# Kernel optimization log

Measured on AMD Instinct MI355X. Metric: run time of the kernel, lower is better.

The kernel has to match this reference:

```python
import jax, jax.numpy as jnp
import numpy as np

RING_SIZE = 4
SEGMENT_LEN = 1024
DILATION_RATE = 2
EPS = 1e-8


def setup_inputs() -> dict:
    key = jax.random.key(0)
    kq, kk, kv = jax.random.split(key, 3)
    shape = (1, 4096, 16, 64)  # (b, n, h, d)
    q = jax.random.normal(kq, shape, dtype=jnp.float32)
    k = jax.random.normal(kk, shape, dtype=jnp.float32)
    v = jax.random.normal(kv, shape, dtype=jnp.float32)
    return {"q": q, "k": k, "v": v}


def _gather_dilated_chunks(k_local, v_local, chunk_size):
    """Replicate the ring loop: rank 0, dist not initialized -> KV chunk is
    always the local chunk; only the dilation offset varies per ring step.
    Returns concatenated dilated K, V of total length ring_size*chunk_size."""
    ks, vs = [], []
    base = jnp.arange(chunk_size)
    for step in range(RING_SIZE):
        chunk_rank = (-step) % RING_SIZE
        chunk_start = chunk_rank * chunk_size
        offset = (chunk_start // SEGMENT_LEN) % DILATION_RATE
        if DILATION_RATE == 1:
            idx = base
        else:
            idx = (base * DILATION_RATE + offset) % chunk_size
        ks.append(k_local[:, idx])
        vs.append(v_local[:, idx])
    return jnp.concatenate(ks, axis=1), jnp.concatenate(vs, axis=1)


def reference(q, k, v):
    b, n, h, d = q.shape
    chunk_size = n // RING_SIZE
    k_local = k[:, :chunk_size]  # rank 0 local chunk
    v_local = v[:, :chunk_size]
    K, V = _gather_dilated_chunks(k_local, v_local, chunk_size)  # (b, n, h, d)

    # Online softmax over ring steps is mathematically a single stable softmax
    # over the concatenation of all chunk scores, with +1e-8 on sum_exp.
    scale = 1.0 / jnp.sqrt(jnp.asarray(d, dtype=q.dtype))
    scores = jnp.einsum("bqhd,bkhd->bhqk", q, K) * scale  # (b, h, n, n)
    m = jnp.max(scores, axis=-1, keepdims=True)
    p = jnp.exp(scores - m)
    denom = jnp.sum(p, axis=-1, keepdims=True) + EPS  # (b, h, q, 1)
    out = jnp.einsum("bhqk,bkhd->bqhd", p, V)  # (b, q, h, d)
    out = out / jnp.transpose(denom, (0, 2, 1, 3))  # -> (b, q, h, 1)
    return out
```

## Files before the change

kernel.cpp:

```cpp
#include <hip/hip_runtime.h>


typedef __attribute__((ext_vector_type(8))) _Float16 f16x8;
typedef __attribute__((ext_vector_type(2))) __fp16   h16x2;
typedef __attribute__((ext_vector_type(4))) float    f32x4;
typedef __attribute__((ext_vector_type(4))) int      i32x4;

constexpr int HEADS = 16;
constexpr int NQ    = 4096;
constexpr int NK    = 1024;
constexpr int KB    = 64;
constexpr int NT    = NK / KB;
constexpr int NTW   = NT / 2;

constexpr int IMG_K  = 0;
constexpr int IMG_V  = 8192;
constexpr int IMG_SZ = 16384;

constexpr float KSCALE = 0.18033688011112042f;
constexpr float CINIT  = -2.8853900817779268f;

__global__ __launch_bounds__(256)
void prepass(const float* __restrict__ kg, const float* __restrict__ vg,
             char* __restrict__ ws)
{
    const int kt = blockIdx.x;
    const int h  = blockIdx.y;
    const int kb = kt * KB;
    char* img = ws + (size_t)(h * NT + kt) * IMG_SZ;
    const int tid = threadIdx.x;

    #pragma unroll
    for (int i = 0; i < 2; ++i) {
        int u = i * 256 + tid;
        int f = u >> 6, l = u & 63;
        int t = f >> 1, cc = f & 1;
        int g = l >> 4, c = l & 15;
        const float* src = kg + (size_t)(kb + 16 * t + c) * 1024 + h * 64 + 32 * cc + 8 * g;
        float4 a = *(const float4*)src;
        float4 b = *(const float4*)(src + 4);
        f16x8 kk;
        kk[0] = (_Float16)(a.x * KSCALE); kk[1] = (_Float16)(a.y * KSCALE);
        kk[2] = (_Float16)(a.z * KSCALE); kk[3] = (_Float16)(a.w * KSCALE);
        kk[4] = (_Float16)(b.x * KSCALE); kk[5] = (_Float16)(b.y * KSCALE);
        kk[6] = (_Float16)(b.z * KSCALE); kk[7] = (_Float16)(b.w * KSCALE);
        *(f16x8*)(img + IMG_K + u * 16) = kk;
    }

    #pragma unroll
    for (int i = 0; i < 2; ++i) {
        int u = i * 256 + tid;
        int f = u >> 6, l = u & 63;
        int m = f >> 2, td = f & 3;
        int g = l >> 4, c = l & 15;
        f16x8 vv;
        #pragma unroll
        for (int e = 0; e < 8; ++e) {
            int key = kb + 32 * m + 16 * (e >> 2) + 4 * g + (e & 3);
            vv[e] = (_Float16)vg[(size_t)key * 1024 + h * 64 + 16 * td + c];
        }
        *(f16x8*)(img + IMG_V + u * 16) = vv;
    }
}

__global__ __launch_bounds__(128, 2)
void ring_attn_v24(const float* __restrict__ qg,
                   const char* __restrict__ ws,
                   float* __restrict__ outg)
{
    __shared__ __align__(16) float Ob[64 * 68 + 64];

    const int bid  = blockIdx.x;
    const int xcd  = bid & 7;
    const int slot = bid >> 3;
    const int h    = xcd * 2 + (slot >> 6);
    const int qw   = slot & 63;

    const int tid  = threadIdx.x;
    const int w    = tid >> 6;
    const int lane = tid & 63;
    const int g    = lane >> 4;
    const int c    = lane & 15;
    const int qbase = qw * 64;

    const int rot  = ((bid >> 3) ^ (w << 2)) & 7;

    f16x8 qf[4][2];
    #pragma unroll
    for (int H = 0; H < 4; ++H)
        #pragma unroll
        for (int cc = 0; cc < 2; ++cc) {
            const float* src = qg + (size_t)(qbase + 16 * H + c) * 1024 + h * 64 + 32 * cc + 8 * g;
            float4 a = *(const float4*)src;
            float4 b = *(const float4*)(src + 4);
            f16x8 qq;
            qq[0] = (_Float16)a.x; qq[1] = (_Float16)a.y;
            qq[2] = (_Float16)a.z; qq[3] = (_Float16)a.w;
            qq[4] = (_Float16)b.x; qq[5] = (_Float16)b.y;
            qq[6] = (_Float16)b.z; qq[7] = (_Float16)b.w;
            qf[H][cc] = qq;
        }

    const f32x4 cinit = {CINIT, CINIT, CINIT, CINIT};
    const h16x2 ones2 = {(__fp16)1.f, (__fp16)1.f};

    f32x4 o[4][4];
    #pragma unroll
    for (int H = 0; H < 4; ++H)
        #pragma unroll
        for (int td = 0; td < 4; ++td)
            #pragma unroll
            for (int r = 0; r < 4; ++r) o[H][td][r] = 0.f;
    float lac[4] = {0.f, 0.f, 0.f, 0.f};

    const char* himg = ws + (size_t)h * NT * IMG_SZ + lane * 16;

    #pragma unroll
    for (int i = 0; i < NTW; ++i) {
        const int kt = w * NTW + ((i + rot) & 7);
        const char* img = himg + (size_t)kt * IMG_SZ;

        f16x8 kv[8];
        #pragma unroll
        for (int f = 0; f < 8; ++f)
            kv[f] = *(const f16x8*)(img + IMG_K + f * 1024);

        f32x4 s0[4], s1[4], s2[4], s3[4];
        unsigned int wv[4][4][2];
        __builtin_amdgcn_s_setprio(1);
        #pragma unroll
        for (int t = 0; t < 4; ++t) {
            s0[t] = __builtin_amdgcn_mfma_f32_16x16x32_f16(kv[2 * t],     qf[0][0], cinit, 0, 0, 0);
            s0[t] = __builtin_amdgcn_mfma_f32_16x16x32_f16(kv[2 * t + 1], qf[0][1], s0[t], 0, 0, 0);
            s1[t] = __builtin_amdgcn_mfma_f32_16x16x32_f16(kv[2 * t],     qf[1][0], cinit, 0, 0, 0);
            s1[t] = __builtin_amdgcn_mfma_f32_16x16x32_f16(kv[2 * t + 1], qf[1][1], s1[t], 0, 0, 0);
        }
        __builtin_amdgcn_s_setprio(0);
        #pragma unroll
        for (int t = 0; t < 4; ++t) {
            float p0 = __builtin_amdgcn_exp2f(s0[t][0]);
            float p1 = __builtin_amdgcn_exp2f(s0[t][1]);
            float p2 = __builtin_amdgcn_exp2f(s0[t][2]);
            float p3 = __builtin_amdgcn_exp2f(s0[t][3]);
            h16x2 w0 = __builtin_amdgcn_cvt_pkrtz(p0, p1);
            h16x2 w1 = __builtin_amdgcn_cvt_pkrtz(p2, p3);
            lac[0] = __builtin_amdgcn_fdot2(w0, ones2, lac[0], false);
            lac[0] = __builtin_amdgcn_fdot2(w1, ones2, lac[0], false);
            wv[0][t][0] = __builtin_bit_cast(unsigned int, w0);
            wv[0][t][1] = __builtin_bit_cast(unsigned int, w1);
        }
        #pragma unroll
        for (int t = 0; t < 4; ++t) {
            float p0 = __builtin_amdgcn_exp2f(s1[t][0]);
            float p1 = __builtin_amdgcn_exp2f(s1[t][1]);
            float p2 = __builtin_amdgcn_exp2f(s1[t][2]);
            float p3 = __builtin_amdgcn_exp2f(s1[t][3]);
            h16x2 w0 = __builtin_amdgcn_cvt_pkrtz(p0, p1);
            h16x2 w1 = __builtin_amdgcn_cvt_pkrtz(p2, p3);
            lac[1] = __builtin_amdgcn_fdot2(w0, ones2, lac[1], false);
            lac[1] = __builtin_amdgcn_fdot2(w1, ones2, lac[1], false);
            wv[1][t][0] = __builtin_bit_cast(unsigned int, w0);
            wv[1][t][1] = __builtin_bit_cast(unsigned int, w1);
        }

        __builtin_amdgcn_s_setprio(1);
        #pragma unroll
        for (int t = 0; t < 4; ++t) {
            s2[t] = __builtin_amdgcn_mfma_f32_16x16x32_f16(kv[2 * t],     qf[2][0], cinit, 0, 0, 0);
            s2[t] = __builtin_amdgcn_mfma_f32_16x16x32_f16(kv[2 * t + 1], qf[2][1], s2[t], 0, 0, 0);
            s3[t] = __builtin_amdgcn_mfma_f32_16x16x32_f16(kv[2 * t],     qf[3][0], cinit, 0, 0, 0);
            s3[t] = __builtin_amdgcn_mfma_f32_16x16x32_f16(kv[2 * t + 1], qf[3][1], s3[t], 0, 0, 0);
        }
        __builtin_amdgcn_s_setprio(0);

        #pragma unroll
        for (int f = 0; f < 8; ++f)
            kv[f] = *(const f16x8*)(img + IMG_V + f * 1024);

        #pragma unroll
        for (int t = 0; t < 4; ++t) {
            float p0 = __builtin_amdgcn_exp2f(s2[t][0]);
            float p1 = __builtin_amdgcn_exp2f(s2[t][1]);
            float p2 = __builtin_amdgcn_exp2f(s2[t][2]);
            float p3 = __builtin_amdgcn_exp2f(s2[t][3]);
            h16x2 w0 = __builtin_amdgcn_cvt_pkrtz(p0, p1);
            h16x2 w1 = __builtin_amdgcn_cvt_pkrtz(p2, p3);
            lac[2] = __builtin_amdgcn_fdot2(w0, ones2, lac[2], false);
            lac[2] = __builtin_amdgcn_fdot2(w1, ones2, lac[2], false);
            wv[2][t][0] = __builtin_bit_cast(unsigned int, w0);
            wv[2][t][1] = __builtin_bit_cast(unsigned int, w1);
        }
        #pragma unroll
        for (int t = 0; t < 4; ++t) {
            float p0 = __builtin_amdgcn_exp2f(s3[t][0]);
            float p1 = __builtin_amdgcn_exp2f(s3[t][1]);
            float p2 = __builtin_amdgcn_exp2f(s3[t][2]);
            float p3 = __builtin_amdgcn_exp2f(s3[t][3]);
            h16x2 w0 = __builtin_amdgcn_cvt_pkrtz(p0, p1);
            h16x2 w1 = __builtin_amdgcn_cvt_pkrtz(p2, p3);
            lac[3] = __builtin_amdgcn_fdot2(w0, ones2, lac[3], false);
            lac[3] = __builtin_amdgcn_fdot2(w1, ones2, lac[3], false);
            wv[3][t][0] = __builtin_bit_cast(unsigned int, w0);
            wv[3][t][1] = __builtin_bit_cast(unsigned int, w1);
        }

        __builtin_amdgcn_s_setprio(1);
        #pragma unroll
        for (int H = 0; H < 4; ++H) {
            i32x4 c0, c1;
            c0[0] = wv[H][0][0]; c0[1] = wv[H][0][1];
            c0[2] = wv[H][1][0]; c0[3] = wv[H][1][1];
            c1[0] = wv[H][2][0]; c1[1] = wv[H][2][1];
            c1[2] = wv[H][3][0]; c1[3] = wv[H][3][1];
            f16x8 B0 = __builtin_bit_cast(f16x8, c0);
            f16x8 B1 = __builtin_bit_cast(f16x8, c1);
            #pragma unroll
            for (int td = 0; td < 4; ++td) {
                o[H][td] = __builtin_amdgcn_mfma_f32_16x16x32_f16(kv[td],     B0, o[H][td], 0, 0, 0);
                o[H][td] = __builtin_amdgcn_mfma_f32_16x16x32_f16(kv[4 + td], B1, o[H][td], 0, 0, 0);
            }
        }
        __builtin_amdgcn_s_setprio(0);
    }

    #pragma unroll
    for (int H = 0; H < 4; ++H) {
        lac[H] += __shfl_xor(lac[H], 16);
        lac[H] += __shfl_xor(lac[H], 32);
    }

    float* Ls = Ob + 64 * 68;
    if (w == 1) {
        #pragma unroll
        for (int H = 0; H < 4; ++H)
            #pragma unroll
            for (int td = 0; td < 4; ++td) {
                float4 st;
                st.x = o[H][td][0]; st.y = o[H][td][1];
                st.z = o[H][td][2]; st.w = o[H][td][3];
                *(float4*)&Ob[(16 * H + c) * 68 + 16 * td + 4 * g] = st;
            }
        if (lane < 16) {
            #pragma unroll
            for (int H = 0; H < 4; ++H) Ls[16 * H + lane] = lac[H];
        }
    }
    __syncthreads();

    if (w == 0) {
        #pragma unroll
        for (int H = 0; H < 4; ++H) {
            float inv = 1.f / (lac[H] + Ls[16 * H + c]);
            #pragma unroll
            for (int td = 0; td < 4; ++td) {
                float4 pb = *(const float4*)&Ob[(16 * H + c) * 68 + 16 * td + 4 * g];
                float4 st;
                st.x = (o[H][td][0] + pb.x) * inv;
                st.y = (o[H][td][1] + pb.y) * inv;
                st.z = (o[H][td][2] + pb.z) * inv;
                st.w = (o[H][td][3] + pb.w) * inv;
                *(float4*)(outg + (size_t)(qbase + 16 * H + c) * 1024 + h * 64 + 16 * td + 4 * g) = st;
            }
        }
    }
}

extern "C" void kernel_launch(void* const* d_in, const int* in_sizes, int n_in,
                              void* d_out, int out_size, void* d_ws, size_t ws_size,
                              hipStream_t stream) {
    const float* q = (const float*)d_in[0];
    const float* k = (const float*)d_in[1];
    const float* v = (const float*)d_in[2];
    float* out = (float*)d_out;
    char* ws = (char*)d_ws;

    prepass<<<dim3(NT, HEADS), dim3(256), 0, stream>>>(k, v, ws);
    ring_attn_v24<<<dim3(1024), dim3(128), 0, stream>>>(q, ws, out);
}
```

Measured before the change: 33.00 us.

## Double-buffer K tiles in LDS via global_load_lds and prefetch V registers

K tiles are streamed into per-wave double-buffered LDS slots with direct global-to-LDS loads issued two tiles ahead, and V tiles are prefetched into registers one iteration ahead. The main loop is no longer unrolled, and all S MFMAs are grouped before the softmax. The goal is to hide global load latency behind compute. It costs 32KB of LDS per block, which may cut occupancy, and adds explicit waitcnt stalls plus extra register pressure from holding the V tile.

```diff
diff --git a/kernel.cpp b/kernel.cpp
--- a/kernel.cpp
+++ b/kernel.cpp
@@ -19,6 +19,12 @@
 
 constexpr float KSCALE = 0.18033688011112042f;
 constexpr float CINIT  = -2.8853900817779268f;
+
+__device__ __forceinline__ void load_lds16(const void* g, void* l) {
+    __builtin_amdgcn_global_load_lds(
+        (const __attribute__((address_space(1))) void*)g,
+        (__attribute__((address_space(3))) void*)l, 16, 0, 0);
+}
 
 __global__ __launch_bounds__(256)
 void prepass(const float* __restrict__ kg, const float* __restrict__ vg,
@@ -64,11 +70,11 @@
 }
 
 __global__ __launch_bounds__(128, 2)
-void ring_attn_v24(const float* __restrict__ qg,
+void ring_attn_v27(const float* __restrict__ qg,
                    const char* __restrict__ ws,
                    float* __restrict__ outg)
 {
-    __shared__ __align__(16) float Ob[64 * 68 + 64];
+    __shared__ __align__(16) char smem[32768];
 
     const int bid  = blockIdx.x;
     const int xcd  = bid & 7;
@@ -114,28 +120,64 @@
     float lac[4] = {0.f, 0.f, 0.f, 0.f};
 
     const char* himg = ws + (size_t)h * NT * IMG_SZ + lane * 16;
-
-    #pragma unroll
+    char* kslot[2] = { smem + (w * 2 + 0) * 8192, smem + (w * 2 + 1) * 8192 };
+
+    {
+        const char* img0 = himg + (size_t)(w * NTW + rot) * IMG_SZ;
+        const char* img1 = himg + (size_t)(w * NTW + ((1 + rot) & 7)) * IMG_SZ;
+        #pragma unroll
+        for (int f = 0; f < 8; ++f)
+            load_lds16(img0 + IMG_K + f * 1024, kslot[0] + f * 1024);
+        #pragma unroll
+        for (int f = 0; f < 8; ++f)
+            load_lds16(img1 + IMG_K + f * 1024, kslot[1] + f * 1024);
+    }
+    f16x8 vb[8];
+    {
+        const char* img0 = himg + (size_t)(w * NTW + rot) * IMG_SZ;
+        #pragma unroll
+        for (int f = 0; f < 8; ++f)
+            vb[f] = *(const f16x8*)(img0 + IMG_V + f * 1024);
+    }
+
+    #pragma unroll 1
     for (int i = 0; i < NTW; ++i) {
-        const int kt = w * NTW + ((i + rot) & 7);
-        const char* img = himg + (size_t)kt * IMG_SZ;
-
-        f16x8 kv[8];
+        asm volatile("s_waitcnt vmcnt(0)" ::: "memory");
+        __builtin_amdgcn_sched_barrier(0);
+
+        f16x8 ka[8];
         #pragma unroll
         for (int f = 0; f < 8; ++f)
-            kv[f] = *(const f16x8*)(img + IMG_K + f * 1024);
+            ka[f] = *(const f16x8*)(kslot[i & 1] + f * 1024 + lane * 16);
 
         f32x4 s0[4], s1[4], s2[4], s3[4];
         unsigned int wv[4][4][2];
         __builtin_amdgcn_s_setprio(1);
         #pragma unroll
         for (int t = 0; t < 4; ++t) {
-            s0[t] = __builtin_amdgcn_mfma_f32_16x16x32_f16(kv[2 * t],     qf[0][0], cinit, 0, 0, 0);
-            s0[t] = __builtin_amdgcn_mfma_f32_16x16x32_f16(kv[2 * t + 1], qf[0][1], s0[t], 0, 0, 0);
-            s1[t] = __builtin_amdgcn_mfma_f32_16x16x32_f16(kv[2 * t],     qf[1][0], cinit, 0, 0, 0);
-            s1[t] = __builtin_amdgcn_mfma_f32_16x16x32_f16(kv[2 * t + 1], qf[1][1], s1[t], 0, 0, 0);
+            s0[t] = __builtin_amdgcn_mfma_f32_16x16x32_f16(ka[2 * t],     qf[0][0], cinit, 0, 0, 0);
+            s0[t] = __builtin_amdgcn_mfma_f32_16x16x32_f16(ka[2 * t + 1], qf[0][1], s0[t], 0, 0, 0);
+            s1[t] = __builtin_amdgcn_mfma_f32_16x16x32_f16(ka[2 * t],     qf[1][0], cinit, 0, 0, 0);
+            s1[t] = __builtin_amdgcn_mfma_f32_16x16x32_f16(ka[2 * t + 1], qf[1][1], s1[t], 0, 0, 0);
+        }
+        #pragma unroll
+        for (int t = 0; t < 4; ++t) {
+            s2[t] = __builtin_amdgcn_mfma_f32_16x16x32_f16(ka[2 * t],     qf[2][0], cinit, 0, 0, 0);
+            s2[t] = __builtin_amdgcn_mfma_f32_16x16x32_f16(ka[2 * t + 1], qf[2][1], s2[t], 0, 0, 0);
+            s3[t] = __builtin_amdgcn_mfma_f32_16x16x32_f16(ka[2 * t],     qf[3][0], cinit, 0, 0, 0);
+            s3[t] = __builtin_amdgcn_mfma_f32_16x16x32_f16(ka[2 * t + 1], qf[3][1], s3[t], 0, 0, 0);
         }
         __builtin_amdgcn_s_setprio(0);
+
+        if (i + 2 < NTW) {
+            asm volatile("s_waitcnt lgkmcnt(0)" ::: "memory");
+            __builtin_amdgcn_sched_barrier(0);
+            const char* imgn = himg + (size_t)(w * NTW + ((i + 2 + rot) & 7)) * IMG_SZ;
+            #pragma unroll
+            for (int f = 0; f < 8; ++f)
+                load_lds16(imgn + IMG_K + f * 1024, kslot[i & 1] + f * 1024);
+        }
+
         #pragma unroll
         for (int t = 0; t < 4; ++t) {
             float p0 = __builtin_amdgcn_exp2f(s0[t][0]);
@@ -162,21 +204,6 @@
             wv[1][t][0] = __builtin_bit_cast(unsigned int, w0);
             wv[1][t][1] = __builtin_bit_cast(unsigned int, w1);
         }
-
-        __builtin_amdgcn_s_setprio(1);
-        #pragma unroll
-        for (int t = 0; t < 4; ++t) {
-            s2[t] = __builtin_amdgcn_mfma_f32_16x16x32_f16(kv[2 * t],     qf[2][0], cinit, 0, 0, 0);
-            s2[t] = __builtin_amdgcn_mfma_f32_16x16x32_f16(kv[2 * t + 1], qf[2][1], s2[t], 0, 0, 0);
-            s3[t] = __builtin_amdgcn_mfma_f32_16x16x32_f16(kv[2 * t],     qf[3][0], cinit, 0, 0, 0);
-            s3[t] = __builtin_amdgcn_mfma_f32_16x16x32_f16(kv[2 * t + 1], qf[3][1], s3[t], 0, 0, 0);
-        }
-        __builtin_amdgcn_s_setprio(0);
-
-        #pragma unroll
-        for (int f = 0; f < 8; ++f)
-            kv[f] = *(const f16x8*)(img + IMG_V + f * 1024);
-
         #pragma unroll
         for (int t = 0; t < 4; ++t) {
             float p0 = __builtin_amdgcn_exp2f(s2[t][0]);
@@ -216,11 +243,18 @@
             f16x8 B1 = __builtin_bit_cast(f16x8, c1);
             #pragma unroll
             for (int td = 0; td < 4; ++td) {
-                o[H][td] = __builtin_amdgcn_mfma_f32_16x16x32_f16(kv[td],     B0, o[H][td], 0, 0, 0);
-                o[H][td] = __builtin_amdgcn_mfma_f32_16x16x32_f16(kv[4 + td], B1, o[H][td], 0, 0, 0);
+                o[H][td] = __builtin_amdgcn_mfma_f32_16x16x32_f16(vb[td],     B0, o[H][td], 0, 0, 0);
+                o[H][td] = __builtin_amdgcn_mfma_f32_16x16x32_f16(vb[4 + td], B1, o[H][td], 0, 0, 0);
             }
         }
         __builtin_amdgcn_s_setprio(0);
+
+        if (i + 1 < NTW) {
+            const char* imgv = himg + (size_t)(w * NTW + ((i + 1 + rot) & 7)) * IMG_SZ;
+            #pragma unroll
+            for (int f = 0; f < 8; ++f)
+                vb[f] = *(const f16x8*)(imgv + IMG_V + f * 1024);
+        }
     }
 
     #pragma unroll
@@ -229,7 +263,9 @@
         lac[H] += __shfl_xor(lac[H], 32);
     }
 
-    float* Ls = Ob + 64 * 68;
+    __syncthreads();
+    float* Ob = (float*)smem;
+    float* Ls = (float*)(smem + 64 * 68 * 4);
     if (w == 1) {
         #pragma unroll
         for (int H = 0; H < 4; ++H)
@@ -275,5 +311,5 @@
     char* ws = (char*)d_ws;
 
     prepass<<<dim3(NT, HEADS), dim3(256), 0, stream>>>(k, v, ws);
-    ring_attn_v24<<<dim3(1024), dim3(128), 0, stream>>>(q, ws, out);
+    ring_attn_v27<<<dim3(1024), dim3(128), 0, stream>>>(q, ws, out);
 }
```

New measurement: 35.73 us. 8.3% more time.
